# Performance work log

Measured on AMD Instinct MI355X. Metric: run time of the kernel, lower is better.

## Reference

```python
import jax, jax.numpy as jnp
import numpy as np

D = 512
E = 1024
LAMBDA_INIT = 0.05

def setup_inputs() -> dict:
    key = jax.random.key(0)
    ks = jax.random.split(key, 8)
    B, S = 4, 4096
    X = jax.random.normal(ks[0], (B, S, E), dtype=jnp.float32)
    Wq = jax.random.normal(ks[1], (2 * D, E), dtype=jnp.float32) / np.sqrt(E)
    bq = jnp.zeros((2 * D,), dtype=jnp.float32)
    Wk = jax.random.normal(ks[2], (2 * D, E), dtype=jnp.float32) / np.sqrt(E)
    bk = jnp.zeros((2 * D,), dtype=jnp.float32)
    Wv = jax.random.normal(ks[3], (D, E), dtype=jnp.float32) / np.sqrt(E)
    bv = jnp.zeros((D,), dtype=jnp.float32)
    lam = jax.random.normal(ks[4], (1,), dtype=jnp.float32)
    return {"X": X, "Wq": Wq, "bq": bq, "Wk": Wk, "bk": bk, "Wv": Wv, "bv": bv, "lam": lam}

def reference(X, Wq, bq, Wk, bk, Wv, bv, lam):
    # Linear projections (torch Linear: x @ W.T + b)
    Q = jnp.einsum('bse,fe->bsf', X, Wq) + bq   # [B,S,2d]
    K = jnp.einsum('bse,fe->bsf', X, Wk) + bk   # [B,S,2d]
    V = jnp.einsum('bse,de->bsd', X, Wv) + bv   # [B,S,d]
    Q1, Q2 = Q[..., :D], Q[..., D:]
    K1, K2 = K[..., :D], K[..., D:]
    s = 1.0 / np.sqrt(D)
    A1 = jnp.einsum('bqd,bkd->bqk', Q1, K1) * s  # [B,S,S]
    A2 = jnp.einsum('bqd,bkd->bqk', Q2, K2) * s
    P1 = jax.nn.softmax(A1, axis=-1)
    P2 = jax.nn.softmax(A2, axis=-1)
    lambda_ = jnp.exp(lam) + LAMBDA_INIT         # scalar [1]
    diff = P1 - lambda_ * P2
    return jnp.einsum('bqk,bkd->bqd', diff, V)   # [B,S,d]
```

## Files before the change

kernel.cpp:

```cpp
#include <hip/hip_runtime.h>
#include <cstdint>
#include <cstddef>

#define NB    4
#define SEQ   4096
#define EDIM  1024
#define DHEAD 512
#define NTOK  (NB * SEQ)
#define FQK   2048
#define FQKV  2560

typedef __bf16 bf16x8 __attribute__((ext_vector_type(8)));
typedef float  f32x4  __attribute__((ext_vector_type(4)));

#define WAITCNT(VM) asm volatile("s_waitcnt vmcnt(" #VM ") lgkmcnt(0)" ::: "memory")
#define BAR() __builtin_amdgcn_s_barrier()

__device__ __forceinline__ unsigned short f2bf(float f) {
  union { float f; unsigned int u; } v; v.f = f;
  return (unsigned short)((v.u + 0x7fffu + ((v.u >> 16) & 1u)) >> 16);
}

__device__ __forceinline__ void gld_lds16(const void* g, void* l) {
  __builtin_amdgcn_global_load_lds(
      (const __attribute__((address_space(1))) unsigned int*)g,
      (__attribute__((address_space(3))) unsigned int*)l, 16, 0, 0);
}

template <class Epi>
__device__ __forceinline__ void gemm_bt_core(
    const unsigned short* __restrict__ A, const unsigned short* __restrict__ B,
    int K, int lda, int ldb, int m0, int n0, Epi epi) {
  __shared__ __align__(16) unsigned short As[2][128 * 32];
  __shared__ __align__(16) unsigned short Bs[2][128 * 32];
  const int t = threadIdx.x;
  const int w = t >> 6;
  const int lane = t & 63;
  const int wr = w >> 1, wc = w & 1;
  const int l15 = lane & 15, c16 = lane >> 4, x3 = l15 & 3;

  f32x4 acc[4][4];
#pragma unroll
  for (int i = 0; i < 4; ++i)
#pragma unroll
    for (int j = 0; j < 4; ++j) acc[i][j] = f32x4{0.f, 0.f, 0.f, 0.f};

  const int c0 = w * 128 + lane;
  const int c1 = w * 128 + 64 + lane;
  const int r0 = c0 >> 2, s0 = (c0 & 3) ^ (r0 & 3);
  const int r1 = c1 >> 2, s1 = (c1 & 3) ^ (r1 & 3);
  const int o0 = (w * 128) * 8;
  const int o1 = (w * 128 + 64) * 8;
  const unsigned short* gA0 = A + (size_t)(m0 + r0) * lda + s0 * 8;
  const unsigned short* gA1 = A + (size_t)(m0 + r1) * lda + s1 * 8;
  const unsigned short* gB0 = B + (size_t)(n0 + r0) * ldb + s0 * 8;
  const unsigned short* gB1 = B + (size_t)(n0 + r1) * ldb + s1 * 8;

  auto STAGE = [&](int buf, int kt) {
    gld_lds16(gA0 + kt, &As[buf][o0]);
    gld_lds16(gA1 + kt, &As[buf][o1]);
    gld_lds16(gB0 + kt, &Bs[buf][o0]);
    gld_lds16(gB1 + kt, &Bs[buf][o1]);
  };

  STAGE(0, 0);
  const int NT = K >> 5;
  for (int tt = 0; tt < NT; ++tt) {
    const int cb = tt & 1;
    if (tt + 1 < NT) { STAGE(cb ^ 1, (tt + 1) * 32); WAITCNT(4); }
    else             { WAITCNT(0); }
    BAR();
    __builtin_amdgcn_s_setprio(1);
    bf16x8 af[4], bfr[4];
#pragma unroll
    for (int tm = 0; tm < 4; ++tm) {
      int r = wr * 64 + tm * 16 + l15;
      af[tm] = *(const bf16x8*)&As[cb][r * 32 + ((c16 ^ x3) * 8)];
    }
#pragma unroll
    for (int tn = 0; tn < 4; ++tn) {
      int r = wc * 64 + tn * 16 + l15;
      bfr[tn] = *(const bf16x8*)&Bs[cb][r * 32 + ((c16 ^ x3) * 8)];
    }
#pragma unroll
    for (int tm = 0; tm < 4; ++tm)
#pragma unroll
      for (int tn = 0; tn < 4; ++tn)
        acc[tm][tn] = __builtin_amdgcn_mfma_f32_16x16x32_bf16(
            af[tm], bfr[tn], acc[tm][tn], 0, 0, 0);
    __builtin_amdgcn_s_setprio(0);
    BAR();
  }
  epi(acc, wr, wc, lane);
}

__global__ void k_cvt_x(const float* __restrict__ X, unsigned short* __restrict__ Xb) {
  int i = blockIdx.x * blockDim.x + threadIdx.x;
  float4 v = ((const float4*)X)[i];
  ushort4 o;
  o.x = f2bf(v.x); o.y = f2bf(v.y); o.z = f2bf(v.z); o.w = f2bf(v.w);
  ((ushort4*)Xb)[i] = o;
}

__global__ void k_pack_w(const float* __restrict__ Wq, const float* __restrict__ Wk,
                         const float* __restrict__ Wv, unsigned short* __restrict__ Wb) {
  int i = blockIdx.x * blockDim.x + threadIdx.x;
  int idx = i * 4;
  int f = idx >> 10, e = idx & 1023;
  const float* src = (f < 1024) ? (Wq + (size_t)f * 1024)
                   : (f < 2048) ? (Wk + (size_t)(f - 1024) * 1024)
                                : (Wv + (size_t)(f - 2048) * 1024);
  float4 v = *(const float4*)(src + e);
  ushort4 o;
  o.x = f2bf(v.x); o.y = f2bf(v.y); o.z = f2bf(v.z); o.w = f2bf(v.w);
  ((ushort4*)Wb)[i] = o;
}

__global__ void k_pack_b(const float* __restrict__ bq, const float* __restrict__ bk,
                         const float* __restrict__ bv, float* __restrict__ bc) {
  int f = blockIdx.x * blockDim.x + threadIdx.x;
  if (f < FQKV)
    bc[f] = (f < 1024) ? bq[f] : (f < 2048) ? bk[f - 1024] : bv[f - 2048];
}

__global__ void k_zero_f(float* __restrict__ p) {
  int i = blockIdx.x * blockDim.x + threadIdx.x;
  p[i] = 0.f;
}

__global__ __launch_bounds__(256) void k_qk(const unsigned short* __restrict__ Xb,
                                            const unsigned short* __restrict__ Wb,
                                            const float* __restrict__ bc,
                                            unsigned short* __restrict__ QK) {
  const int m0 = blockIdx.y * 128, n0 = blockIdx.x * 128;
  gemm_bt_core(Xb, Wb, EDIM, EDIM, EDIM, m0, n0,
    [&](f32x4 (&acc)[4][4], int wr, int wc, int lane) {
#pragma unroll
      for (int tm = 0; tm < 4; ++tm)
#pragma unroll
        for (int tn = 0; tn < 4; ++tn) {
          int kc = n0 + wc * 64 + tn * 16 + (lane & 15);
          float bias = bc[kc];
#pragma unroll
          for (int i = 0; i < 4; ++i) {
            int q = m0 + wr * 64 + tm * 16 + (lane >> 4) * 4 + i;
            __bf16 h = (__bf16)(acc[tm][tn][i] + bias);
            QK[(size_t)q * FQK + kc] = *(const unsigned short*)&h;
          }
        }
    });
}

__global__ __launch_bounds__(256) void k_v(const unsigned short* __restrict__ Xb,
                                           const unsigned short* __restrict__ Wb,
                                           const float* __restrict__ bc,
                                           unsigned short* __restrict__ Vt) {
  const int b = blockIdx.z;
  const int m0 = blockIdx.y * 128;
  const int n0 = blockIdx.x * 128;
  const unsigned short* A = Wb + (size_t)2048 * EDIM;
  const unsigned short* B = Xb + (size_t)b * SEQ * EDIM;
  unsigned short* Vb = Vt + (size_t)b * DHEAD * SEQ;
  gemm_bt_core(A, B, EDIM, EDIM, EDIM, m0, n0,
    [&](f32x4 (&acc)[4][4], int wr, int wc, int lane) {
#pragma unroll
      for (int tm = 0; tm < 4; ++tm)
#pragma unroll
        for (int tn = 0; tn < 4; ++tn) {
          int s = n0 + wc * 64 + tn * 16 + (lane & 15);
#pragma unroll
          for (int i = 0; i < 4; ++i) {
            int d = m0 + wr * 64 + tm * 16 + (lane >> 4) * 4 + i;
            __bf16 h = (__bf16)(acc[tm][tn][i] + bc[2048 + d]);
            Vb[(size_t)d * SEQ + s] = *(const unsigned short*)&h;
          }
        }
    });
}

__global__ __launch_bounds__(512, 2) void k_scores8(const unsigned short* __restrict__ QK,
                                                    unsigned short* __restrict__ E_c,
                                                    float* __restrict__ ls, int b0) {
  __shared__ __align__(16) unsigned short LA[2][256 * 64];
  __shared__ __align__(16) unsigned short LB[2][256 * 64];
  const int z = blockIdx.z, rb = z >> 1, which = z & 1, b = b0 + rb;
  const int m0 = blockIdx.y * 256, n0 = blockIdx.x * 256;
  const unsigned short* Aq = QK + (size_t)b * SEQ * FQK + which * 512;
  const unsigned short* Bk = Aq + 1024;
  unsigned short* Eb = E_c + (size_t)z * SEQ * SEQ;
  float* lr = ls + (size_t)which * NTOK + (size_t)b * SEQ;
  const int t = threadIdx.x, w = t >> 6, lane = t & 63;
  const int wr = w >> 2, wc = w & 3;
  const int l15 = lane & 15, c16 = lane >> 4, x7 = l15 & 7;

  f32x4 acc[8][4];
#pragma unroll
  for (int i = 0; i < 8; ++i)
#pragma unroll
    for (int j = 0; j < 4; ++j) acc[i][j] = f32x4{0.f, 0.f, 0.f, 0.f};

  unsigned goffA[4], goffB[4]; int loff[4];
#pragma unroll
  for (int i = 0; i < 4; ++i) {
    int c = w * 64 + lane + 512 * i;
    int r = c >> 3;
    int sg = (c & 7) ^ (r & 7);
    goffA[i] = (unsigned)((m0 + r) * FQK + sg * 8);
    goffB[i] = (unsigned)((n0 + r) * FQK + sg * 8);
    loff[i] = (w * 64 + 512 * i) * 8;
  }

  auto STAGE = [&](int buf, int kh) {
#pragma unroll
    for (int i = 0; i < 4; ++i) gld_lds16(Aq + goffA[i] + kh, &LA[buf][loff[i]]);
#pragma unroll
    for (int i = 0; i < 4; ++i) gld_lds16(Bk + goffB[i] + kh, &LB[buf][loff[i]]);
  };

  STAGE(0, 0);
  for (int kt = 0; kt < 8; ++kt) {
    const int cb = kt & 1;
    if (kt < 7) { STAGE(cb ^ 1, (kt + 1) * 64); WAITCNT(8); }
    else        { WAITCNT(0); }
    BAR();
    __builtin_amdgcn_s_setprio(1);
    bf16x8 bfr[4][2];
#pragma unroll
    for (int tn = 0; tn < 4; ++tn)
#pragma unroll
      for (int ks = 0; ks < 2; ++ks)
        bfr[tn][ks] = *(const bf16x8*)
            &LB[cb][(wc * 64 + tn * 16 + l15) * 64 + (((ks * 4 + c16) ^ x7) * 8)];
#pragma unroll
    for (int mh = 0; mh < 2; ++mh) {
      bf16x8 af[4][2];
#pragma unroll
      for (int tq = 0; tq < 4; ++tq)
#pragma unroll
        for (int ks = 0; ks < 2; ++ks)
          af[tq][ks] = *(const bf16x8*)
              &LA[cb][(wr * 128 + mh * 64 + tq * 16 + l15) * 64 + (((ks * 4 + c16) ^ x7) * 8)];
#pragma unroll
      for (int tq = 0; tq < 4; ++tq)
#pragma unroll
        for (int tn = 0; tn < 4; ++tn)
#pragma unroll
          for (int ks = 0; ks < 2; ++ks)
            acc[mh * 4 + tq][tn] = __builtin_amdgcn_mfma_f32_16x16x32_bf16(
                af[tq][ks], bfr[tn][ks], acc[mh * 4 + tq][tn], 0, 0, 0);
    }
    __builtin_amdgcn_s_setprio(0);
    BAR();
  }

  const float scale = 0.04419417382415922f;
  float rs[8][4];
#pragma unroll
  for (int tm = 0; tm < 8; ++tm)
#pragma unroll
    for (int i = 0; i < 4; ++i) rs[tm][i] = 0.f;
#pragma unroll
  for (int tm = 0; tm < 8; ++tm)
#pragma unroll
    for (int tn = 0; tn < 4; ++tn) {
      int k = n0 + wc * 64 + tn * 16 + l15;
#pragma unroll
      for (int i = 0; i < 4; ++i) {
        int q = m0 + wr * 128 + tm * 16 + c16 * 4 + i;
        float e = __expf(acc[tm][tn][i] * scale);
        __bf16 h = (__bf16)e;
        Eb[(size_t)q * SEQ + k] = *(const unsigned short*)&h;
        rs[tm][i] += (float)h;
      }
    }
#pragma unroll
  for (int tm = 0; tm < 8; ++tm)
#pragma unroll
    for (int i = 0; i < 4; ++i) {
      float v = rs[tm][i];
      v += __shfl_xor(v, 1);
      v += __shfl_xor(v, 2);
      v += __shfl_xor(v, 4);
      v += __shfl_xor(v, 8);
      rs[tm][i] = v;
    }
  if (l15 == 0) {
#pragma unroll
    for (int tm = 0; tm < 8; ++tm)
#pragma unroll
      for (int i = 0; i < 4; ++i) {
        int q = m0 + wr * 128 + tm * 16 + c16 * 4 + i;
        atomicAdd(&lr[q], rs[tm][i]);
      }
  }
}

__global__ __launch_bounds__(512, 2) void k_pv8(const unsigned short* __restrict__ E_c,
                                                const unsigned short* __restrict__ Vt,
                                                float* __restrict__ O12, int b0) {
  __shared__ __align__(16) unsigned short LA[2][256 * 64];
  __shared__ __align__(16) unsigned short LB[2][128 * 64];
  const int z = blockIdx.z, b = b0 + (z >> 1);
  const int q0 = blockIdx.y * 256, n0 = blockIdx.x * 128;
  const unsigned short* Ae = E_c + (size_t)z * SEQ * SEQ;
  const unsigned short* Bv = Vt + (size_t)b * DHEAD * SEQ;
  float* Ob = O12 + (size_t)z * SEQ * DHEAD;
  const int t = threadIdx.x, w = t >> 6, lane = t & 63;
  const int wr = w >> 1, wc = w & 1;
  const int l15 = lane & 15, c16 = lane >> 4, x7 = l15 & 7;

  f32x4 acc[4][4];
#pragma unroll
  for (int i = 0; i < 4; ++i)
#pragma unroll
    for (int j = 0; j < 4; ++j) acc[i][j] = f32x4{0.f, 0.f, 0.f, 0.f};

  unsigned goffE[4], goffV[2]; int loffE[4], loffV[2];
#pragma unroll
  for (int i = 0; i < 4; ++i) {
    int c = w * 64 + lane + 512 * i;
    int r = c >> 3;
    int sg = (c & 7) ^ (r & 7);
    goffE[i] = (unsigned)((q0 + r) * SEQ + sg * 8);
    loffE[i] = (w * 64 + 512 * i) * 8;
  }
#pragma unroll
  for (int i = 0; i < 2; ++i) {
    int c = w * 64 + lane + 512 * i;
    int r = c >> 3;
    int sg = (c & 7) ^ (r & 7);
    goffV[i] = (unsigned)((n0 + r) * SEQ + sg * 8);
    loffV[i] = (w * 64 + 512 * i) * 8;
  }

  auto STAGE = [&](int buf, int kh) {
#pragma unroll
    for (int i = 0; i < 4; ++i) gld_lds16(Ae + goffE[i] + kh, &LA[buf][loffE[i]]);
#pragma unroll
    for (int i = 0; i < 2; ++i) gld_lds16(Bv + goffV[i] + kh, &LB[buf][loffV[i]]);
  };

  STAGE(0, 0);
  for (int kt = 0; kt < 64; ++kt) {
    const int cb = kt & 1;
    if (kt < 63) { STAGE(cb ^ 1, (kt + 1) * 64); WAITCNT(6); }
    else         { WAITCNT(0); }
    BAR();
    __builtin_amdgcn_s_setprio(1);
    bf16x8 af[4][2], bfr[4][2];
#pragma unroll
    for (int tn = 0; tn < 4; ++tn)
#pragma unroll
      for (int ks = 0; ks < 2; ++ks)
        bfr[tn][ks] = *(const bf16x8*)
            &LB[cb][(wc * 64 + tn * 16 + l15) * 64 + (((ks * 4 + c16) ^ x7) * 8)];
#pragma unroll
    for (int tq = 0; tq < 4; ++tq)
#pragma unroll
      for (int ks = 0; ks < 2; ++ks)
        af[tq][ks] = *(const bf16x8*)
            &LA[cb][(wr * 64 + tq * 16 + l15) * 64 + (((ks * 4 + c16) ^ x7) * 8)];
#pragma unroll
    for (int tq = 0; tq < 4; ++tq)
#pragma unroll
      for (int tn = 0; tn < 4; ++tn)
#pragma unroll
        for (int ks = 0; ks < 2; ++ks)
          acc[tq][tn] = __builtin_amdgcn_mfma_f32_16x16x32_bf16(
              af[tq][ks], bfr[tn][ks], acc[tq][tn], 0, 0, 0);
    __builtin_amdgcn_s_setprio(0);
    BAR();
  }

#pragma unroll
  for (int tq = 0; tq < 4; ++tq)
#pragma unroll
    for (int tn = 0; tn < 4; ++tn) {
      int d = n0 + wc * 64 + tn * 16 + l15;
#pragma unroll
      for (int i = 0; i < 4; ++i) {
        int q = q0 + wr * 64 + tq * 16 + c16 * 4 + i;
        Ob[(size_t)q * DHEAD + d] = acc[tq][tn][i];
      }
    }
}

__global__ void k_combine(const float* __restrict__ O12, const float* __restrict__ ls,
                          const float* __restrict__ lam, float* __restrict__ out, int b0) {
  int i = blockIdx.x * blockDim.x + threadIdx.x;
  float lambda = expf(lam[0]) + 0.05f;
  int gq = i >> 7;
  int rb = gq >> 12;
  int q = gq & 4095;
  int dv = i & 127;
  int b = b0 + rb;
  float inv1 = 1.f / ls[(size_t)b * SEQ + q];
  float inv2 = lambda / ls[NTOK + (size_t)b * SEQ + q];
  size_t ai = (size_t)(rb * 2) * (SEQ * 128) + (size_t)q * 128 + dv;
  float4 a = ((const float4*)O12)[ai];
  float4 c = ((const float4*)O12)[ai + SEQ * 128];
  float4 r;
  r.x = a.x * inv1 - c.x * inv2;
  r.y = a.y * inv1 - c.y * inv2;
  r.z = a.z * inv1 - c.z * inv2;
  r.w = a.w * inv1 - c.w * inv2;
  ((float4*)out)[(size_t)(b * SEQ + q) * 128 + dv] = r;
}

extern "C" void kernel_launch(void* const* d_in, const int* in_sizes, int n_in,
                              void* d_out, int out_size, void* d_ws, size_t ws_size,
                              hipStream_t stream) {
  const float* X   = (const float*)d_in[0];
  const float* Wq  = (const float*)d_in[1];
  const float* bq  = (const float*)d_in[2];
  const float* Wk  = (const float*)d_in[3];
  const float* bk  = (const float*)d_in[4];
  const float* Wv  = (const float*)d_in[5];
  const float* bv  = (const float*)d_in[6];
  const float* lam = (const float*)d_in[7];
  float* out = (float*)d_out;

  char* ws = (char*)d_ws;
  size_t off = 0;
  auto alloc = [&](size_t b) { size_t r = off; off += (b + 255) & ~(size_t)255; return r; };
  unsigned short* Xb  = (unsigned short*)(ws + alloc((size_t)NTOK * EDIM * 2));
  unsigned short* Wb  = (unsigned short*)(ws + alloc((size_t)FQKV * EDIM * 2));
  float*          bc  = (float*)(ws + alloc((size_t)FQKV * 4));
  unsigned short* QK  = (unsigned short*)(ws + alloc((size_t)NTOK * FQK * 2));
  unsigned short* Vt  = (unsigned short*)(ws + alloc((size_t)NB * DHEAD * SEQ * 2));
  unsigned short* E_c = (unsigned short*)(ws + alloc((size_t)4 * SEQ * SEQ * 2));
  float*          ls  = (float*)(ws + alloc((size_t)2 * NTOK * 4));
  float* O12 = (float*)Xb;

  k_cvt_x<<<dim3((NTOK * EDIM / 4) / 256), dim3(256), 0, stream>>>(X, Xb);
  k_pack_w<<<dim3((FQKV * EDIM / 4) / 256), dim3(256), 0, stream>>>(Wq, Wk, Wv, Wb);
  k_pack_b<<<dim3(10), dim3(256), 0, stream>>>(bq, bk, bv, bc);
  k_qk<<<dim3(FQK / 128, NTOK / 128), dim3(256), 0, stream>>>(Xb, Wb, bc, QK);
  k_v<<<dim3(SEQ / 128, DHEAD / 128, NB), dim3(256), 0, stream>>>(Xb, Wb, bc, Vt);
  k_zero_f<<<dim3(2 * NTOK / 256), dim3(256), 0, stream>>>(ls);
  for (int b0 = 0; b0 < NB; b0 += 2) {
    k_scores8<<<dim3(SEQ / 256, SEQ / 256, 4), dim3(512), 0, stream>>>(QK, E_c, ls, b0);
    k_pv8<<<dim3(DHEAD / 128, SEQ / 256, 4), dim3(512), 0, stream>>>(E_c, Vt, O12, b0);
    k_combine<<<dim3((2 * SEQ * DHEAD / 4) / 256), dim3(256), 0, stream>>>(O12, ls, lam, out, b0);
  }

  (void)in_sizes; (void)n_in; (void)out_size; (void)ws_size;
}
```

Before: 689.8 us.

## Split score and PV GEMM main loops into ping-pong phases of LDS reads and MFMA

Restructures the K-loop of the score GEMM and the P·V GEMM so that each iteration issues the next-tile global→LDS prefetch first. It then alternates phases of LDS fragment reads and MFMA clusters separated by barriers, sched_barrier and priority toggles, in the style of a ping-pong schedule between waves. The goal is to overlap LDS traffic of one wave with the matrix work of another and to cut register pressure by loading B fragments in halves. In exchange the loop has several more barriers per iteration and waits for the full prefetch at the end of each iteration, which can serialize memory latency.

```diff
diff --git a/kernel.cpp b/kernel.cpp
--- a/kernel.cpp
+++ b/kernel.cpp
@@ -14,7 +14,11 @@
 typedef float  f32x4  __attribute__((ext_vector_type(4)));
 
 #define WAITCNT(VM) asm volatile("s_waitcnt vmcnt(" #VM ") lgkmcnt(0)" ::: "memory")
-#define BAR() __builtin_amdgcn_s_barrier()
+#define LGKM0()     asm volatile("s_waitcnt lgkmcnt(0)" ::: "memory")
+#define SCHED0()    __builtin_amdgcn_sched_barrier(0)
+#define BAR()       __builtin_amdgcn_s_barrier()
+#define PRIO1()     __builtin_amdgcn_s_setprio(1)
+#define PRIO0()     __builtin_amdgcn_s_setprio(0)
 
 __device__ __forceinline__ unsigned short f2bf(float f) {
   union { float f; unsigned int u; } v; v.f = f;
@@ -70,7 +74,7 @@
     if (tt + 1 < NT) { STAGE(cb ^ 1, (tt + 1) * 32); WAITCNT(4); }
     else             { WAITCNT(0); }
     BAR();
-    __builtin_amdgcn_s_setprio(1);
+    PRIO1();
     bf16x8 af[4], bfr[4];
 #pragma unroll
     for (int tm = 0; tm < 4; ++tm) {
@@ -88,7 +92,7 @@
       for (int tn = 0; tn < 4; ++tn)
         acc[tm][tn] = __builtin_amdgcn_mfma_f32_16x16x32_bf16(
             af[tm], bfr[tn], acc[tm][tn], 0, 0, 0);
-    __builtin_amdgcn_s_setprio(0);
+    PRIO0();
     BAR();
   }
   epi(acc, wr, wc, lane);
@@ -217,41 +221,88 @@
     for (int i = 0; i < 4; ++i) gld_lds16(Bk + goffB[i] + kh, &LB[buf][loff[i]]);
   };
 
+#define LDA_S(CB, R, KS) (*(const bf16x8*)&LA[CB][(R) * 64 + ((((KS) * 4 + c16) ^ x7) * 8)])
+#define LDB_S(CB, R, KS) (*(const bf16x8*)&LB[CB][(R) * 64 + ((((KS) * 4 + c16) ^ x7) * 8)])
+
   STAGE(0, 0);
+  WAITCNT(0);
+  BAR();
+
   for (int kt = 0; kt < 8; ++kt) {
     const int cb = kt & 1;
-    if (kt < 7) { STAGE(cb ^ 1, (kt + 1) * 64); WAITCNT(8); }
-    else        { WAITCNT(0); }
-    BAR();
-    __builtin_amdgcn_s_setprio(1);
-    bf16x8 bfr[4][2];
-#pragma unroll
-    for (int tn = 0; tn < 4; ++tn)
-#pragma unroll
-      for (int ks = 0; ks < 2; ++ks)
-        bfr[tn][ks] = *(const bf16x8*)
-            &LB[cb][(wc * 64 + tn * 16 + l15) * 64 + (((ks * 4 + c16) ^ x7) * 8)];
-#pragma unroll
-    for (int mh = 0; mh < 2; ++mh) {
-      bf16x8 af[4][2];
-#pragma unroll
-      for (int tq = 0; tq < 4; ++tq)
+    bf16x8 af[4][2], b0f[2][2], b1f[2][2];
+    if (kt < 7) STAGE(cb ^ 1, (kt + 1) * 64);
+#pragma unroll
+    for (int tq = 0; tq < 4; ++tq)
+#pragma unroll
+      for (int ks = 0; ks < 2; ++ks)
+        af[tq][ks] = LDA_S(cb, wr * 128 + tq * 16 + l15, ks);
+#pragma unroll
+    for (int tn = 0; tn < 2; ++tn)
+#pragma unroll
+      for (int ks = 0; ks < 2; ++ks)
+        b0f[tn][ks] = LDB_S(cb, wc * 64 + tn * 16 + l15, ks);
+    BAR(); LGKM0(); SCHED0();
+    PRIO1();
+#pragma unroll
+    for (int tq = 0; tq < 4; ++tq)
+#pragma unroll
+      for (int tn = 0; tn < 2; ++tn)
 #pragma unroll
         for (int ks = 0; ks < 2; ++ks)
-          af[tq][ks] = *(const bf16x8*)
-              &LA[cb][(wr * 128 + mh * 64 + tq * 16 + l15) * 64 + (((ks * 4 + c16) ^ x7) * 8)];
-#pragma unroll
-      for (int tq = 0; tq < 4; ++tq)
-#pragma unroll
-        for (int tn = 0; tn < 4; ++tn)
-#pragma unroll
-          for (int ks = 0; ks < 2; ++ks)
-            acc[mh * 4 + tq][tn] = __builtin_amdgcn_mfma_f32_16x16x32_bf16(
-                af[tq][ks], bfr[tn][ks], acc[mh * 4 + tq][tn], 0, 0, 0);
-    }
-    __builtin_amdgcn_s_setprio(0);
-    BAR();
-  }
+          acc[tq][tn] = __builtin_amdgcn_mfma_f32_16x16x32_bf16(
+              af[tq][ks], b0f[tn][ks], acc[tq][tn], 0, 0, 0);
+    PRIO0();
+    BAR();
+#pragma unroll
+    for (int tn = 0; tn < 2; ++tn)
+#pragma unroll
+      for (int ks = 0; ks < 2; ++ks)
+        b1f[tn][ks] = LDB_S(cb, wc * 64 + (tn + 2) * 16 + l15, ks);
+    BAR(); LGKM0(); SCHED0();
+    PRIO1();
+#pragma unroll
+    for (int tq = 0; tq < 4; ++tq)
+#pragma unroll
+      for (int tn = 0; tn < 2; ++tn)
+#pragma unroll
+        for (int ks = 0; ks < 2; ++ks)
+          acc[tq][tn + 2] = __builtin_amdgcn_mfma_f32_16x16x32_bf16(
+              af[tq][ks], b1f[tn][ks], acc[tq][tn + 2], 0, 0, 0);
+    PRIO0();
+    BAR();
+#pragma unroll
+    for (int tq = 0; tq < 4; ++tq)
+#pragma unroll
+      for (int ks = 0; ks < 2; ++ks)
+        af[tq][ks] = LDA_S(cb, wr * 128 + 64 + tq * 16 + l15, ks);
+    BAR(); LGKM0(); SCHED0();
+    PRIO1();
+#pragma unroll
+    for (int tq = 0; tq < 4; ++tq)
+#pragma unroll
+      for (int tn = 0; tn < 2; ++tn)
+#pragma unroll
+        for (int ks = 0; ks < 2; ++ks)
+          acc[4 + tq][tn + 2] = __builtin_amdgcn_mfma_f32_16x16x32_bf16(
+              af[tq][ks], b1f[tn][ks], acc[4 + tq][tn + 2], 0, 0, 0);
+    PRIO0();
+    BAR();
+    PRIO1();
+#pragma unroll
+    for (int tq = 0; tq < 4; ++tq)
+#pragma unroll
+      for (int tn = 0; tn < 2; ++tn)
+#pragma unroll
+        for (int ks = 0; ks < 2; ++ks)
+          acc[4 + tq][tn] = __builtin_amdgcn_mfma_f32_16x16x32_bf16(
+              af[tq][ks], b0f[tn][ks], acc[4 + tq][tn], 0, 0, 0);
+    PRIO0();
+    if (kt < 7) WAITCNT(0);
+    BAR();
+  }
+#undef LDA_S
+#undef LDB_S
 
   const float scale = 0.04419417382415922f;
   float rs[8][4];
@@ -340,37 +391,60 @@
     for (int i = 0; i < 2; ++i) gld_lds16(Bv + goffV[i] + kh, &LB[buf][loffV[i]]);
   };
 
+#define LDA_P(CB, R, KS) (*(const bf16x8*)&LA[CB][(R) * 64 + ((((KS) * 4 + c16) ^ x7) * 8)])
+#define LDB_P(CB, R, KS) (*(const bf16x8*)&LB[CB][(R) * 64 + ((((KS) * 4 + c16) ^ x7) * 8)])
+
   STAGE(0, 0);
+  WAITCNT(0);
+  BAR();
+
   for (int kt = 0; kt < 64; ++kt) {
     const int cb = kt & 1;
-    if (kt < 63) { STAGE(cb ^ 1, (kt + 1) * 64); WAITCNT(6); }
-    else         { WAITCNT(0); }
-    BAR();
-    __builtin_amdgcn_s_setprio(1);
-    bf16x8 af[4][2], bfr[4][2];
-#pragma unroll
-    for (int tn = 0; tn < 4; ++tn)
-#pragma unroll
-      for (int ks = 0; ks < 2; ++ks)
-        bfr[tn][ks] = *(const bf16x8*)
-            &LB[cb][(wc * 64 + tn * 16 + l15) * 64 + (((ks * 4 + c16) ^ x7) * 8)];
-#pragma unroll
-    for (int tq = 0; tq < 4; ++tq)
-#pragma unroll
-      for (int ks = 0; ks < 2; ++ks)
-        af[tq][ks] = *(const bf16x8*)
-            &LA[cb][(wr * 64 + tq * 16 + l15) * 64 + (((ks * 4 + c16) ^ x7) * 8)];
-#pragma unroll
-    for (int tq = 0; tq < 4; ++tq)
-#pragma unroll
-      for (int tn = 0; tn < 4; ++tn)
+    bf16x8 af[4][2], b0f[2][2], b1f[2][2];
+    if (kt < 63) STAGE(cb ^ 1, (kt + 1) * 64);
+#pragma unroll
+    for (int tq = 0; tq < 4; ++tq)
+#pragma unroll
+      for (int ks = 0; ks < 2; ++ks)
+        af[tq][ks] = LDA_P(cb, wr * 64 + tq * 16 + l15, ks);
+#pragma unroll
+    for (int tn = 0; tn < 2; ++tn)
+#pragma unroll
+      for (int ks = 0; ks < 2; ++ks)
+        b0f[tn][ks] = LDB_P(cb, wc * 64 + tn * 16 + l15, ks);
+    BAR(); LGKM0(); SCHED0();
+    PRIO1();
+#pragma unroll
+    for (int tq = 0; tq < 4; ++tq)
+#pragma unroll
+      for (int tn = 0; tn < 2; ++tn)
 #pragma unroll
         for (int ks = 0; ks < 2; ++ks)
           acc[tq][tn] = __builtin_amdgcn_mfma_f32_16x16x32_bf16(
-              af[tq][ks], bfr[tn][ks], acc[tq][tn], 0, 0, 0);
-    __builtin_amdgcn_s_setprio(0);
-    BAR();
-  }
+              af[tq][ks], b0f[tn][ks], acc[tq][tn], 0, 0, 0);
+    PRIO0();
+    BAR();
+#pragma unroll
+    for (int tn = 0; tn < 2; ++tn)
+#pragma unroll
+      for (int ks = 0; ks < 2; ++ks)
+        b1f[tn][ks] = LDB_P(cb, wc * 64 + (tn + 2) * 16 + l15, ks);
+    BAR(); LGKM0(); SCHED0();
+    PRIO1();
+#pragma unroll
+    for (int tq = 0; tq < 4; ++tq)
+#pragma unroll
+      for (int tn = 0; tn < 2; ++tn)
+#pragma unroll
+        for (int ks = 0; ks < 2; ++ks)
+          acc[tq][tn + 2] = __builtin_amdgcn_mfma_f32_16x16x32_bf16(
+              af[tq][ks], b1f[tn][ks], acc[tq][tn + 2], 0, 0, 0);
+    PRIO0();
+    if (kt < 63) WAITCNT(0);
+    BAR();
+  }
+#undef LDA_P
+#undef LDB_P
 
 #pragma unroll
   for (int tq = 0; tq < 4; ++tq)
```

Measured after the change: 734.1 us. 6.4% more time.

## Fuse PV matmuls for both heads with combine epilogue

Applied to the files above, without the earlier changes.

Replaces the separate P·V kernel and the combine kernel with one kernel. Each block computes both heads' E·V products for a 128x128 output tile, sharing the V tile in LDS, and writes the lambda-weighted normalized difference straight to the output. This removes the O12 intermediate round-trip and a launch, and loads V once for both heads. In exchange the q tile shrinks from 256 to 128, so E reuse per V load changes, and the output stores are scalar rather than float4.

```diff
diff --git a/kernel.cpp b/kernel.cpp
--- a/kernel.cpp
+++ b/kernel.cpp
@@ -14,7 +14,9 @@
 typedef float  f32x4  __attribute__((ext_vector_type(4)));
 
 #define WAITCNT(VM) asm volatile("s_waitcnt vmcnt(" #VM ") lgkmcnt(0)" ::: "memory")
-#define BAR() __builtin_amdgcn_s_barrier()
+#define BAR()       __builtin_amdgcn_s_barrier()
+#define PRIO1()     __builtin_amdgcn_s_setprio(1)
+#define PRIO0()     __builtin_amdgcn_s_setprio(0)
 
 __device__ __forceinline__ unsigned short f2bf(float f) {
   union { float f; unsigned int u; } v; v.f = f;
@@ -70,7 +72,7 @@
     if (tt + 1 < NT) { STAGE(cb ^ 1, (tt + 1) * 32); WAITCNT(4); }
     else             { WAITCNT(0); }
     BAR();
-    __builtin_amdgcn_s_setprio(1);
+    PRIO1();
     bf16x8 af[4], bfr[4];
 #pragma unroll
     for (int tm = 0; tm < 4; ++tm) {
@@ -88,7 +90,7 @@
       for (int tn = 0; tn < 4; ++tn)
         acc[tm][tn] = __builtin_amdgcn_mfma_f32_16x16x32_bf16(
             af[tm], bfr[tn], acc[tm][tn], 0, 0, 0);
-    __builtin_amdgcn_s_setprio(0);
+    PRIO0();
     BAR();
   }
   epi(acc, wr, wc, lane);
@@ -223,7 +225,7 @@
     if (kt < 7) { STAGE(cb ^ 1, (kt + 1) * 64); WAITCNT(8); }
     else        { WAITCNT(0); }
     BAR();
-    __builtin_amdgcn_s_setprio(1);
+    PRIO1();
     bf16x8 bfr[4][2];
 #pragma unroll
     for (int tn = 0; tn < 4; ++tn)
@@ -249,7 +251,7 @@
             acc[mh * 4 + tq][tn] = __builtin_amdgcn_mfma_f32_16x16x32_bf16(
                 af[tq][ks], bfr[tn][ks], acc[mh * 4 + tq][tn], 0, 0, 0);
     }
-    __builtin_amdgcn_s_setprio(0);
+    PRIO0();
     BAR();
   }
 
@@ -295,49 +297,52 @@
   }
 }
 
-__global__ __launch_bounds__(512, 2) void k_pv8(const unsigned short* __restrict__ E_c,
+__global__ __launch_bounds__(512, 2) void k_pvc(const unsigned short* __restrict__ E_c,
                                                 const unsigned short* __restrict__ Vt,
-                                                float* __restrict__ O12, int b0) {
-  __shared__ __align__(16) unsigned short LA[2][256 * 64];
-  __shared__ __align__(16) unsigned short LB[2][128 * 64];
-  const int z = blockIdx.z, b = b0 + (z >> 1);
-  const int q0 = blockIdx.y * 256, n0 = blockIdx.x * 128;
-  const unsigned short* Ae = E_c + (size_t)z * SEQ * SEQ;
+                                                const float* __restrict__ ls,
+                                                const float* __restrict__ lam,
+                                                float* __restrict__ out, int b0) {
+  __shared__ __align__(16) unsigned short LE1[2][128 * 64];
+  __shared__ __align__(16) unsigned short LE2[2][128 * 64];
+  __shared__ __align__(16) unsigned short LV[2][128 * 64];
+  const int z = blockIdx.z;
+  const int b = b0 + z;
+  const int q0 = blockIdx.y * 128, n0 = blockIdx.x * 128;
+  const unsigned short* E1 = E_c + (size_t)(z * 2 + 0) * SEQ * SEQ;
+  const unsigned short* E2 = E_c + (size_t)(z * 2 + 1) * SEQ * SEQ;
   const unsigned short* Bv = Vt + (size_t)b * DHEAD * SEQ;
-  float* Ob = O12 + (size_t)z * SEQ * DHEAD;
   const int t = threadIdx.x, w = t >> 6, lane = t & 63;
-  const int wr = w >> 1, wc = w & 1;
+  const int wq = w & 1, wd = w >> 1;
   const int l15 = lane & 15, c16 = lane >> 4, x7 = l15 & 7;
 
-  f32x4 acc[4][4];
+  f32x4 acc1[4][2], acc2[4][2];
 #pragma unroll
   for (int i = 0; i < 4; ++i)
 #pragma unroll
-    for (int j = 0; j < 4; ++j) acc[i][j] = f32x4{0.f, 0.f, 0.f, 0.f};
-
-  unsigned goffE[4], goffV[2]; int loffE[4], loffV[2];
-#pragma unroll
-  for (int i = 0; i < 4; ++i) {
-    int c = w * 64 + lane + 512 * i;
-    int r = c >> 3;
-    int sg = (c & 7) ^ (r & 7);
-    goffE[i] = (unsigned)((q0 + r) * SEQ + sg * 8);
-    loffE[i] = (w * 64 + 512 * i) * 8;
-  }
+    for (int j = 0; j < 2; ++j) {
+      acc1[i][j] = f32x4{0.f, 0.f, 0.f, 0.f};
+      acc2[i][j] = f32x4{0.f, 0.f, 0.f, 0.f};
+    }
+
+  unsigned goffE1[2], goffE2[2], goffV[2]; int loff[2];
 #pragma unroll
   for (int i = 0; i < 2; ++i) {
     int c = w * 64 + lane + 512 * i;
     int r = c >> 3;
     int sg = (c & 7) ^ (r & 7);
-    goffV[i] = (unsigned)((n0 + r) * SEQ + sg * 8);
-    loffV[i] = (w * 64 + 512 * i) * 8;
+    goffE1[i] = (unsigned)((q0 + r) * SEQ + sg * 8);
+    goffE2[i] = goffE1[i];
+    goffV[i]  = (unsigned)((n0 + r) * SEQ + sg * 8);
+    loff[i] = (w * 64 + 512 * i) * 8;
   }
 
   auto STAGE = [&](int buf, int kh) {
 #pragma unroll
-    for (int i = 0; i < 4; ++i) gld_lds16(Ae + goffE[i] + kh, &LA[buf][loffE[i]]);
-#pragma unroll
-    for (int i = 0; i < 2; ++i) gld_lds16(Bv + goffV[i] + kh, &LB[buf][loffV[i]]);
+    for (int i = 0; i < 2; ++i) gld_lds16(E1 + goffE1[i] + kh, &LE1[buf][loff[i]]);
+#pragma unroll
+    for (int i = 0; i < 2; ++i) gld_lds16(E2 + goffE2[i] + kh, &LE2[buf][loff[i]]);
+#pragma unroll
+    for (int i = 0; i < 2; ++i) gld_lds16(Bv + goffV[i] + kh, &LV[buf][loff[i]]);
   };
 
   STAGE(0, 0);
@@ -346,65 +351,52 @@
     if (kt < 63) { STAGE(cb ^ 1, (kt + 1) * 64); WAITCNT(6); }
     else         { WAITCNT(0); }
     BAR();
-    __builtin_amdgcn_s_setprio(1);
-    bf16x8 af[4][2], bfr[4][2];
-#pragma unroll
-    for (int tn = 0; tn < 4; ++tn)
+    PRIO1();
+    bf16x8 a1[4][2], a2[4][2], bfr[2][2];
+#pragma unroll
+    for (int tn = 0; tn < 2; ++tn)
 #pragma unroll
       for (int ks = 0; ks < 2; ++ks)
         bfr[tn][ks] = *(const bf16x8*)
-            &LB[cb][(wc * 64 + tn * 16 + l15) * 64 + (((ks * 4 + c16) ^ x7) * 8)];
+            &LV[cb][(wd * 32 + tn * 16 + l15) * 64 + (((ks * 4 + c16) ^ x7) * 8)];
 #pragma unroll
     for (int tq = 0; tq < 4; ++tq)
 #pragma unroll
-      for (int ks = 0; ks < 2; ++ks)
-        af[tq][ks] = *(const bf16x8*)
-            &LA[cb][(wr * 64 + tq * 16 + l15) * 64 + (((ks * 4 + c16) ^ x7) * 8)];
+      for (int ks = 0; ks < 2; ++ks) {
+        int r = (wq * 64 + tq * 16 + l15) * 64 + (((ks * 4 + c16) ^ x7) * 8);
+        a1[tq][ks] = *(const bf16x8*)&LE1[cb][r];
+        a2[tq][ks] = *(const bf16x8*)&LE2[cb][r];
+      }
 #pragma unroll
     for (int tq = 0; tq < 4; ++tq)
 #pragma unroll
-      for (int tn = 0; tn < 4; ++tn)
-#pragma unroll
-        for (int ks = 0; ks < 2; ++ks)
-          acc[tq][tn] = __builtin_amdgcn_mfma_f32_16x16x32_bf16(
-              af[tq][ks], bfr[tn][ks], acc[tq][tn], 0, 0, 0);
-    __builtin_amdgcn_s_setprio(0);
-    BAR();
-  }
-
+      for (int tn = 0; tn < 2; ++tn)
+#pragma unroll
+        for (int ks = 0; ks < 2; ++ks) {
+          acc1[tq][tn] = __builtin_amdgcn_mfma_f32_16x16x32_bf16(
+              a1[tq][ks], bfr[tn][ks], acc1[tq][tn], 0, 0, 0);
+          acc2[tq][tn] = __builtin_amdgcn_mfma_f32_16x16x32_bf16(
+              a2[tq][ks], bfr[tn][ks], acc2[tq][tn], 0, 0, 0);
+        }
+    PRIO0();
+    BAR();
+  }
+
+  const float lambda = __expf(lam[0]) + 0.05f;
 #pragma unroll
   for (int tq = 0; tq < 4; ++tq)
 #pragma unroll
-    for (int tn = 0; tn < 4; ++tn) {
-      int d = n0 + wc * 64 + tn * 16 + l15;
+    for (int tn = 0; tn < 2; ++tn) {
+      int d = n0 + wd * 32 + tn * 16 + l15;
 #pragma unroll
       for (int i = 0; i < 4; ++i) {
-        int q = q0 + wr * 64 + tq * 16 + c16 * 4 + i;
-        Ob[(size_t)q * DHEAD + d] = acc[tq][tn][i];
+        int q = q0 + wq * 64 + tq * 16 + c16 * 4 + i;
+        float inv1 = 1.f / ls[(size_t)b * SEQ + q];
+        float inv2 = lambda / ls[NTOK + (size_t)b * SEQ + q];
+        out[((size_t)(b * SEQ + q)) * DHEAD + d] =
+            acc1[tq][tn][i] * inv1 - acc2[tq][tn][i] * inv2;
       }
     }
-}
-
-__global__ void k_combine(const float* __restrict__ O12, const float* __restrict__ ls,
-                          const float* __restrict__ lam, float* __restrict__ out, int b0) {
-  int i = blockIdx.x * blockDim.x + threadIdx.x;
-  float lambda = expf(lam[0]) + 0.05f;
-  int gq = i >> 7;
-  int rb = gq >> 12;
-  int q = gq & 4095;
-  int dv = i & 127;
-  int b = b0 + rb;
-  float inv1 = 1.f / ls[(size_t)b * SEQ + q];
-  float inv2 = lambda / ls[NTOK + (size_t)b * SEQ + q];
-  size_t ai = (size_t)(rb * 2) * (SEQ * 128) + (size_t)q * 128 + dv;
-  float4 a = ((const float4*)O12)[ai];
-  float4 c = ((const float4*)O12)[ai + SEQ * 128];
-  float4 r;
-  r.x = a.x * inv1 - c.x * inv2;
-  r.y = a.y * inv1 - c.y * inv2;
-  r.z = a.z * inv1 - c.z * inv2;
-  r.w = a.w * inv1 - c.w * inv2;
-  ((float4*)out)[(size_t)(b * SEQ + q) * 128 + dv] = r;
 }
 
 extern "C" void kernel_launch(void* const* d_in, const int* in_sizes, int n_in,
@@ -430,7 +422,6 @@
   unsigned short* Vt  = (unsigned short*)(ws + alloc((size_t)NB * DHEAD * SEQ * 2));
   unsigned short* E_c = (unsigned short*)(ws + alloc((size_t)4 * SEQ * SEQ * 2));
   float*          ls  = (float*)(ws + alloc((size_t)2 * NTOK * 4));
-  float* O12 = (float*)Xb;
 
   k_cvt_x<<<dim3((NTOK * EDIM / 4) / 256), dim3(256), 0, stream>>>(X, Xb);
   k_pack_w<<<dim3((FQKV * EDIM / 4) / 256), dim3(256), 0, stream>>>(Wq, Wk, Wv, Wb);
@@ -440,8 +431,7 @@
   k_zero_f<<<dim3(2 * NTOK / 256), dim3(256), 0, stream>>>(ls);
   for (int b0 = 0; b0 < NB; b0 += 2) {
     k_scores8<<<dim3(SEQ / 256, SEQ / 256, 4), dim3(512), 0, stream>>>(QK, E_c, ls, b0);
-    k_pv8<<<dim3(DHEAD / 128, SEQ / 256, 4), dim3(512), 0, stream>>>(E_c, Vt, O12, b0);
-    k_combine<<<dim3((2 * SEQ * DHEAD / 4) / 256), dim3(256), 0, stream>>>(O12, ls, lam, out, b0);
+    k_pvc<<<dim3(DHEAD / 128, SEQ / 128, 2), dim3(512), 0, stream>>>(E_c, Vt, ls, lam, out, b0);
   }
 
   (void)in_sizes; (void)n_in; (void)out_size; (void)ws_size;
```

After: 724.3 us. +5.0%, slower.
